# Performance work log

Measured on AMD Instinct MI355X. Metric: run time of the kernel, lower is better.

Reference implementation:

```python
import jax, jax.numpy as jnp
import numpy as np

DIM = 512
HID = 512
H = 8
HD = HID // H
RB_HID = 64
COORD = 3


def setup_inputs() -> dict:
    key = jax.random.key(0)
    ks = jax.random.split(key, 12)
    B, Nq, Nk = 2, 1024, 2048
    s = 0.02
    return {
        "q_in": jax.random.normal(ks[0], (B, Nq, DIM), jnp.float32),
        "kv_in": jax.random.normal(ks[1], (B, Nk, DIM), jnp.float32),
        "q_coords": jax.random.normal(ks[2], (B, Nq, COORD), jnp.float32),
        "kv_coords": jax.random.normal(ks[3], (B, Nk, COORD), jnp.float32),
        "Wq": jax.random.normal(ks[4], (DIM, HID), jnp.float32) * s,
        "Wk": jax.random.normal(ks[5], (DIM, HID), jnp.float32) * s,
        "Wv": jax.random.normal(ks[6], (DIM, HID), jnp.float32) * s,
        "Wo": jax.random.normal(ks[7], (HID, DIM), jnp.float32) * s,
        "W1": jax.random.normal(ks[8], (1, RB_HID), jnp.float32) * s,
        "b1": jnp.zeros((RB_HID,), jnp.float32),
        "W2": jax.random.normal(ks[9], (RB_HID, H), jnp.float32) * s,
        "b2": jnp.zeros((H,), jnp.float32),
    }


def reference(q_in, kv_in, q_coords, kv_coords, Wq, Wk, Wv, Wo, W1, b1, W2, b2):
    B, Nq, _ = q_in.shape
    Nk = kv_in.shape[1]
    # projections -> [B, H, N, HD]
    q = (q_in @ Wq).reshape(B, Nq, H, HD).transpose(0, 2, 1, 3)
    k = (kv_in @ Wk).reshape(B, Nk, H, HD).transpose(0, 2, 1, 3)
    v = (kv_in @ Wv).reshape(B, Nk, H, HD).transpose(0, 2, 1, 3)
    # pairwise Euclidean distance [B, Nq, Nk]
    diff = q_coords[:, :, None, :] - kv_coords[:, None, :, :]
    d = jnp.sqrt(jnp.sum(diff * diff, axis=-1))
    # 2-layer MLP on distance -> per-head bias [B, H, Nq, Nk]
    h = jax.nn.silu(d[..., None] * W1[0] + b1)  # [B,Nq,Nk,RB_HID]
    bias = (h @ W2 + b2).transpose(0, 3, 1, 2)  # [B,H,Nq,Nk]
    scale = HD ** -0.5
    logits = jnp.einsum("bhqd,bhkd->bhqk", q, k) * scale + bias
    attn = jax.nn.softmax(logits, axis=-1)
    out = jnp.einsum("bhqk,bhkd->bhqd", attn, v)
    out = out.transpose(0, 2, 1, 3).reshape(B, Nq, HID)
    return out @ Wo
```

## Files before the change

### kernel.cpp

```cpp
#include <hip/hip_runtime.h>
#include <hip/hip_bf16.h>
#include <math.h>

typedef short bf16x8 __attribute__((ext_vector_type(8)));
typedef float f32x4 __attribute__((ext_vector_type(4)));
typedef unsigned short u16;
typedef unsigned int u32;

#define NH 8
#define BB 2
#define NQ 1024
#define NK 2048
#define M2CONST 6.4921250
#define SC2 0.18033688f

#define MFMA16(a, b, c) __builtin_amdgcn_mfma_f32_16x16x32_bf16(a, b, c, 0, 0, 0)

__device__ __constant__ double XN_D[6] = {15.727406610312546, 13.656854249492380,
                                          10.070552360820166, 5.9294476391798335,
                                          2.3431457505076194, 0.27259338968745405};
#define XN0 15.727406610312546f
#define XN1 13.656854249492380f
#define XN2 10.070552360820166f
#define XN3 5.9294476391798335f
#define XN4 2.3431457505076194f

static __device__ __forceinline__ u16 f2us(float x) {
  union { __hip_bfloat16 b; u16 u; } cv;
  cv.b = __float2bfloat16(x);
  return cv.u;
}

static __device__ __forceinline__ u32 bfr(float x) {
  u32 u = __builtin_bit_cast(u32, x);
  return u + 0x7FFFu + ((u >> 16) & 1u);
}
static __device__ __forceinline__ u32 pk2(float lo, float hi) {
  return (bfr(lo) >> 16) | (bfr(hi) & 0xFFFF0000u);
}
static __device__ __forceinline__ u16 bfs(float x) { return (u16)(bfr(x) >> 16); }

static __device__ __forceinline__ bf16x8 pack8(float4 a, float4 b) {
  union { bf16x8 v; uint4 u; } cv;
  cv.u.x = pk2(a.x, a.y);
  cv.u.y = pk2(a.z, a.w);
  cv.u.z = pk2(b.x, b.y);
  cv.u.w = pk2(b.z, b.w);
  return cv.v;
}

__global__ __launch_bounds__(256) void setup_kernel(
    const float* __restrict__ Wq, const float* __restrict__ Wk,
    const float* __restrict__ Wv, const float* __restrict__ Wo,
    u16* __restrict__ Tq, u16* __restrict__ Tk,
    u16* __restrict__ Tv, u16* __restrict__ To,
    const float* __restrict__ W1, const float* __restrict__ b1,
    const float* __restrict__ W2, const float* __restrict__ b2,
    float* __restrict__ polyc,
    const float* __restrict__ kc, u16* __restrict__ keg) {
  const int blk = blockIdx.x, t = threadIdx.x;
  if (blk < 256) {
    __shared__ u16 tile[64][65];
    const float* W; u16* Wt;
    switch (blk >> 6) {
      case 0: W = Wq; Wt = Tq; break;
      case 1: W = Wk; Wt = Tk; break;
      case 2: W = Wv; Wt = Tv; break;
      default: W = Wo; Wt = To; break;
    }
    const int rem = blk & 63;
    const int k0 = (rem >> 3) * 64, n0 = (rem & 7) * 64;
    const int r = t >> 4, c4 = (t & 15) * 4;
    #pragma unroll
    for (int p = 0; p < 4; p++) {
      int row = p * 16 + r;
      float4 v = *(const float4*)&W[(size_t)(k0 + row) * 512 + n0 + c4];
      tile[row][c4 + 0] = f2us(v.x);
      tile[row][c4 + 1] = f2us(v.y);
      tile[row][c4 + 2] = f2us(v.z);
      tile[row][c4 + 3] = f2us(v.w);
    }
    __syncthreads();
    #pragma unroll
    for (int p = 0; p < 4; p++) {
      int n = p * 16 + r;
      u16 u0 = tile[c4 + 0][n], u1 = tile[c4 + 1][n];
      u16 u2 = tile[c4 + 2][n], u3 = tile[c4 + 3][n];
      uint2 o;
      o.x = u0 | ((u32)u1 << 16);
      o.y = u2 | ((u32)u3 << 16);
      *(uint2*)&Wt[(size_t)(n0 + n) * 512 + k0 + c4] = o;
    }
  } else if (blk == 256) {
    __shared__ double fv[6][8];
    if (t < 48) {
      int i = t >> 3, h = t & 7;
      double x = XN_D[i];
      double acc = (double)b2[h];
      for (int r = 0; r < 64; r++) {
        double u = x * (double)W1[r] + (double)b1[r];
        double s = u / (1.0 + exp(-u));
        acc += s * (double)W2[r * 8 + h];
      }
      fv[i][h] = acc * 1.4426950408889634 - M2CONST;
    }
    __syncthreads();
    if (t < 8) {
      int h = t;
      double c[6];
      #pragma unroll
      for (int i = 0; i < 6; i++) c[i] = fv[i][h];
      for (int k = 1; k < 6; k++)
        for (int i = 5; i >= k; i--)
          c[i] = (c[i] - c[i - 1]) / (XN_D[i] - XN_D[i - k]);
      #pragma unroll
      for (int j = 0; j < 6; j++) polyc[h * 8 + j] = (float)c[j];
    }
  } else {
    int r = (blk - 257) * 256 + t;
    float kx = kc[(size_t)r * 3], ky = kc[(size_t)r * 3 + 1], kz = kc[(size_t)r * 3 + 2];
    uint4 o;
    o.x = f2us(-2.0f * kx) | ((u32)f2us(-2.0f * ky) << 16);
    o.y = f2us(-2.0f * kz) | ((u32)f2us(1.0f) << 16);
    o.z = (u32)f2us(kx * kx + ky * ky + kz * kz);
    o.w = 0;
    *(uint4*)&keg[(size_t)r * 8] = o;
  }
}

__global__ __launch_bounds__(256) void gemm_qkv(
    const float* __restrict__ q_in, const float* __restrict__ kv_in,
    const u16* __restrict__ Wqt, const u16* __restrict__ Wkt,
    const u16* __restrict__ Wvt, u16* __restrict__ Qp,
    u16* __restrict__ Kp, u16* __restrict__ Vtp) {
  __shared__ u16 As[64 * 72];
  __shared__ u16 Bs[64 * 72];
  __shared__ u16 Bs2[64 * 72];
  const int t = threadIdx.x;
  const int w = t >> 6, l = t & 63, g = l >> 4, li = l & 15;
  const int bx = blockIdx.x;
  const bool isQ = bx < 32;
  const int m0 = (isQ ? bx : bx - 32) * 64, n0 = blockIdx.y * 64;
  const float* A = isQ ? q_in : kv_in;
  const u16* B1 = isQ ? Wqt : Wkt;
  const int ms = (w & 1) * 32, ns = (w >> 1) * 32;
  const int ar = t >> 2, ac = (t & 3) * 16;
  f32x4 acc[2][2] = {}, accV[2][2] = {};

  for (int kt = 0; kt < 512; kt += 64) {
    float4 a4[4];
    #pragma unroll
    for (int q = 0; q < 4; q++)
      a4[q] = *(const float4*)&A[(size_t)(m0 + ar) * 512 + kt + ac + 4 * q];
    bf16x8 bk[2], bv2[2];
    #pragma unroll
    for (int p = 0; p < 2; p++) {
      int f = p * 256 + t, r = f >> 3, c8 = (f & 7) * 8;
      bk[p] = *(const bf16x8*)&B1[(size_t)(n0 + r) * 512 + kt + c8];
    }
    if (!isQ) {
      #pragma unroll
      for (int p = 0; p < 2; p++) {
        int f = p * 256 + t, r = f >> 3, c8 = (f & 7) * 8;
        bv2[p] = *(const bf16x8*)&Wvt[(size_t)(n0 + r) * 512 + kt + c8];
      }
    }
    __syncthreads();
    *(bf16x8*)&As[ar * 72 + ac] = pack8(a4[0], a4[1]);
    *(bf16x8*)&As[ar * 72 + ac + 8] = pack8(a4[2], a4[3]);
    #pragma unroll
    for (int p = 0; p < 2; p++) {
      int f = p * 256 + t, r = f >> 3, c8 = (f & 7) * 8;
      *(bf16x8*)&Bs[r * 72 + c8] = bk[p];
    }
    if (!isQ) {
      #pragma unroll
      for (int p = 0; p < 2; p++) {
        int f = p * 256 + t, r = f >> 3, c8 = (f & 7) * 8;
        *(bf16x8*)&Bs2[r * 72 + c8] = bv2[p];
      }
    }
    __syncthreads();
    #pragma unroll
    for (int ks = 0; ks < 2; ks++) {
      bf16x8 a0 = *(const bf16x8*)&As[(ms + li) * 72 + ks * 32 + g * 8];
      bf16x8 a1 = *(const bf16x8*)&As[(ms + 16 + li) * 72 + ks * 32 + g * 8];
      bf16x8 k0 = *(const bf16x8*)&Bs[(ns + li) * 72 + ks * 32 + g * 8];
      bf16x8 k1 = *(const bf16x8*)&Bs[(ns + 16 + li) * 72 + ks * 32 + g * 8];
      acc[0][0] = MFMA16(a0, k0, acc[0][0]);
      acc[0][1] = MFMA16(a0, k1, acc[0][1]);
      acc[1][0] = MFMA16(a1, k0, acc[1][0]);
      acc[1][1] = MFMA16(a1, k1, acc[1][1]);
      if (!isQ) {
        bf16x8 v0 = *(const bf16x8*)&Bs2[(ns + li) * 72 + ks * 32 + g * 8];
        bf16x8 v1 = *(const bf16x8*)&Bs2[(ns + 16 + li) * 72 + ks * 32 + g * 8];
        accV[0][0] = MFMA16(a0, v0, accV[0][0]);
        accV[0][1] = MFMA16(a0, v1, accV[0][1]);
        accV[1][0] = MFMA16(a1, v0, accV[1][0]);
        accV[1][1] = MFMA16(a1, v1, accV[1][1]);
      }
    }
  }
  #pragma unroll
  for (int mi = 0; mi < 2; mi++) {
    #pragma unroll
    for (int ni = 0; ni < 2; ni++) {
      int row = m0 + ms + mi * 16 + 4 * g;
      int col = n0 + ns + ni * 16 + li;
      f32x4 vk = acc[mi][ni];
      if (isQ) {
        #pragma unroll
        for (int r = 0; r < 4; r++) Qp[(size_t)(row + r) * 512 + col] = bfs(vk[r]);
      } else {
        #pragma unroll
        for (int r = 0; r < 4; r++) Kp[(size_t)(row + r) * 512 + col] = bfs(vk[r]);
        f32x4 vv = accV[mi][ni];
        int bb = row >> 11, j = row & 2047;
        int hh = col >> 6, d = col & 63;
        uint2 o;
        o.x = pk2(vv[0], vv[1]);
        o.y = pk2(vv[2], vv[3]);
        *(uint2*)&Vtp[((size_t)((bb * 8 + hh) * 64 + d)) * 2048 + j] = o;
      }
    }
  }
}

__global__ __launch_bounds__(256, 4) void attn_kernel(
    const u16* __restrict__ Qb, const u16* __restrict__ Kb,
    const u16* __restrict__ Vt, const float* __restrict__ qc,
    const u16* __restrict__ keg, const float* __restrict__ polyc,
    float* __restrict__ Op, float* __restrict__ Lp) {
  __shared__ u16 Kl[64 * 72];
  __shared__ u16 Vtl[64 * 72];
  __shared__ u16 Pl[64 * 72];

  const int t = threadIdx.x;
  const int w = t >> 6, l = t & 63, g = l >> 4, li = l & 15;
  const int qt = blockIdx.x >> 2, sidx = blockIdx.x & 3;
  const int h = blockIdx.y, b = blockIdx.z;

  const float c0 = polyc[h * 8 + 0], c1 = polyc[h * 8 + 1];
  const float c2 = polyc[h * 8 + 2], c3 = polyc[h * 8 + 3];
  const float c4 = polyc[h * 8 + 4], c5 = polyc[h * 8 + 5];

  const int qrow = qt * 64 + w * 16 + li;
  const size_t qg = (size_t)b * NQ + qrow;
  bf16x8 qf0 = *(const bf16x8*)&Qb[qg * 512 + h * 64 + g * 8];
  bf16x8 qf1 = *(const bf16x8*)&Qb[qg * 512 + h * 64 + 32 + g * 8];
  float qx = qc[qg * 3], qy = qc[qg * 3 + 1], qz = qc[qg * 3 + 2];
  bf16x8 qe = {};
  if (g == 0) {
    qe[0] = (short)f2us(qx);
    qe[1] = (short)f2us(qy);
    qe[2] = (short)f2us(qz);
    qe[3] = (short)f2us(qx * qx + qy * qy + qz * qz);
    qe[4] = (short)f2us(1.0f);
  }

  f32x4 oacc[4] = {};
  float lacc = 0.0f;

  const u16* Kg = Kb + (size_t)b * NK * 512 + h * 64;
  const u16* Vg = Vt + (size_t)((b * 8 + h) * 64) * 2048;
  const u16* keg_b = keg + (size_t)b * NK * 8;

  for (int it = 0; it < 8; it++) {
    const int jbase = sidx * 512 + it * 64;
    __syncthreads();
    #pragma unroll
    for (int pp = 0; pp < 2; pp++) {
      int f = pp * 256 + t, row = f >> 3, c8 = (f & 7) * 8;
      *(bf16x8*)&Kl[row * 72 + c8] =
          *(const bf16x8*)&Kg[(size_t)(jbase + row) * 512 + c8];
      *(bf16x8*)&Vtl[row * 72 + c8] =
          *(const bf16x8*)&Vg[(size_t)row * 2048 + jbase + c8];
    }
    __syncthreads();

    f32x4 sac[4], dac[4];
    #pragma unroll
    for (int j4 = 0; j4 < 4; j4++) {
      bf16x8 ka0 = *(const bf16x8*)&Kl[(j4 * 16 + li) * 72 + g * 8];
      bf16x8 ka1 = *(const bf16x8*)&Kl[(j4 * 16 + li) * 72 + 32 + g * 8];
      f32x4 z = {};
      f32x4 s0 = MFMA16(ka0, qf0, z);
      sac[j4] = MFMA16(ka1, qf1, s0);
      bf16x8 ke = {};
      if (g == 0)
        ke = *(const bf16x8*)&keg_b[(size_t)(jbase + j4 * 16 + li) * 8];
      dac[j4] = MFMA16(ke, qe, z);
    }

    #pragma unroll
    for (int j4 = 0; j4 < 4; j4++) {
      float p[4];
      #pragma unroll
      for (int r = 0; r < 4; r++) {
        float u = fmaxf(dac[j4][r], 0.0f);
        float d = fminf(__builtin_amdgcn_sqrtf(u), 16.0f);
        float gp = c5;
        gp = fmaf(gp, d - XN4, c4);
        gp = fmaf(gp, d - XN3, c3);
        gp = fmaf(gp, d - XN2, c2);
        gp = fmaf(gp, d - XN1, c1);
        gp = fmaf(gp, d - XN0, c0);
        p[r] = __builtin_amdgcn_exp2f(fmaf(sac[j4][r], SC2, gp));
        lacc += p[r];
      }
      uint2 pv;
      pv.x = pk2(p[0], p[1]);
      pv.y = pk2(p[2], p[3]);
      *(uint2*)&Pl[(w * 16 + li) * 72 + j4 * 16 + g * 4] = pv;
    }

    bf16x8 pf0 = *(const bf16x8*)&Pl[(w * 16 + li) * 72 + g * 8];
    bf16x8 pf1 = *(const bf16x8*)&Pl[(w * 16 + li) * 72 + 32 + g * 8];
    #pragma unroll
    for (int dt = 0; dt < 4; dt++) {
      bf16x8 v0 = *(const bf16x8*)&Vtl[(dt * 16 + li) * 72 + g * 8];
      bf16x8 v1 = *(const bf16x8*)&Vtl[(dt * 16 + li) * 72 + 32 + g * 8];
      oacc[dt] = MFMA16(pf0, v0, oacc[dt]);
      oacc[dt] = MFMA16(pf1, v1, oacc[dt]);
    }
  }

  float lf = lacc;
  lf += __shfl_xor(lf, 16);
  lf += __shfl_xor(lf, 32);

  const size_t obase =
      ((size_t)(sidx * 16 + b * 8 + h) * 1024 + qt * 64 + w * 16) * 64;
  #pragma unroll
  for (int dt = 0; dt < 4; dt++)
    #pragma unroll
    for (int r = 0; r < 4; r++)
      Op[obase + (size_t)(4 * g + r) * 64 + dt * 16 + li] = oacc[dt][r];
  if (g == 0)
    Lp[(size_t)(sidx * 16 + b * 8 + h) * 1024 + qt * 64 + w * 16 + li] = lf;
}

__global__ __launch_bounds__(256) void gemm_wo(const float* __restrict__ Op,
                                               const float* __restrict__ Lp,
                                               const u16* __restrict__ Bt,
                                               float* __restrict__ C) {
  __shared__ u16 As[32 * 72];
  __shared__ u16 Bs[64 * 72];
  const int t = threadIdx.x;
  const int w = t >> 6, l = t & 63, g = l >> 4, li = l & 15;
  const int m0 = blockIdx.x * 32, n0 = blockIdx.y * 64;
  const int ms = (w & 1) * 16, ns = (w >> 1) * 32;
  const int arow = t >> 3, ac8 = (t & 7) * 8;
  const int bq = (m0 + arow) >> 10, qrow = (m0 + arow) & 1023;
  f32x4 acc[2] = {};

  for (int kt = 0; kt < 512; kt += 64) {
    const int h = kt >> 6;
    const int bh = bq * 8 + h;
    f32x4 s0 = {}, s1 = {};
    float lsum = 0.0f;
    #pragma unroll
    for (int s = 0; s < 4; s++) {
      const float* base = &Op[((size_t)(s * 16 + bh) * 1024 + qrow) * 64 + ac8];
      s0 += *(const f32x4*)base;
      s1 += *(const f32x4*)(base + 4);
      lsum += Lp[(size_t)(s * 16 + bh) * 1024 + qrow];
    }
    float inv = __builtin_amdgcn_rcpf(lsum);
    bf16x8 bv[2];
    #pragma unroll
    for (int p = 0; p < 2; p++) {
      int f = p * 256 + t, r = f >> 3, c8 = (f & 7) * 8;
      bv[p] = *(const bf16x8*)&Bt[(size_t)(n0 + r) * 512 + kt + c8];
    }
    __syncthreads();
    {
      union { bf16x8 v; uint4 u; } cv;
      cv.u.x = pk2(s0[0] * inv, s0[1] * inv);
      cv.u.y = pk2(s0[2] * inv, s0[3] * inv);
      cv.u.z = pk2(s1[0] * inv, s1[1] * inv);
      cv.u.w = pk2(s1[2] * inv, s1[3] * inv);
      *(bf16x8*)&As[arow * 72 + ac8] = cv.v;
    }
    #pragma unroll
    for (int p = 0; p < 2; p++) {
      int f = p * 256 + t, r = f >> 3, c8 = (f & 7) * 8;
      *(bf16x8*)&Bs[r * 72 + c8] = bv[p];
    }
    __syncthreads();
    #pragma unroll
    for (int ks = 0; ks < 2; ks++) {
      bf16x8 af = *(const bf16x8*)&As[(ms + li) * 72 + ks * 32 + g * 8];
      bf16x8 b0 = *(const bf16x8*)&Bs[(ns + li) * 72 + ks * 32 + g * 8];
      bf16x8 b1 = *(const bf16x8*)&Bs[(ns + 16 + li) * 72 + ks * 32 + g * 8];
      acc[0] = MFMA16(af, b0, acc[0]);
      acc[1] = MFMA16(af, b1, acc[1]);
    }
  }
  #pragma unroll
  for (int ni = 0; ni < 2; ni++) {
    f32x4 v = acc[ni];
    int row = m0 + ms + 4 * g;
    int col = n0 + ns + ni * 16 + li;
    #pragma unroll
    for (int r = 0; r < 4; r++) C[(size_t)(row + r) * 512 + col] = v[r];
  }
}

extern "C" void kernel_launch(void* const* d_in, const int* in_sizes, int n_in,
                              void* d_out, int out_size, void* d_ws, size_t ws_size,
                              hipStream_t stream) {
  const float* q_in      = (const float*)d_in[0];
  const float* kv_in     = (const float*)d_in[1];
  const float* q_coords  = (const float*)d_in[2];
  const float* kv_coords = (const float*)d_in[3];
  const float* Wq        = (const float*)d_in[4];
  const float* Wk        = (const float*)d_in[5];
  const float* Wv        = (const float*)d_in[6];
  const float* Wo        = (const float*)d_in[7];
  const float* W1        = (const float*)d_in[8];
  const float* b1        = (const float*)d_in[9];
  const float* W2        = (const float*)d_in[10];
  const float* b2        = (const float*)d_in[11];

  char* p = (char*)d_ws;
  u16* Wqt  = (u16*)p; p += (size_t)512 * 512 * 2;
  u16* Wkt  = (u16*)p; p += (size_t)512 * 512 * 2;
  u16* Wvt  = (u16*)p; p += (size_t)512 * 512 * 2;
  u16* Wot  = (u16*)p; p += (size_t)512 * 512 * 2;
  u16* Qp   = (u16*)p; p += (size_t)2048 * 512 * 2;
  u16* Kp   = (u16*)p; p += (size_t)4096 * 512 * 2;
  u16* Vtp  = (u16*)p; p += (size_t)4096 * 512 * 2;
  u16* keg  = (u16*)p; p += (size_t)4096 * 8 * 2;
  float* polyc = (float*)p; p += (size_t)64 * 4;
  p = (char*)(((size_t)p + 255) & ~(size_t)255);
  float* Opart = (float*)p; p += (size_t)4 * 16 * 1024 * 64 * 4;
  float* Lpart = (float*)p; p += (size_t)4 * 16 * 1024 * 4;

  setup_kernel<<<273, 256, 0, stream>>>(Wq, Wk, Wv, Wo, Wqt, Wkt, Wvt, Wot,
                                        W1, b1, W2, b2, polyc, kv_coords, keg);
  gemm_qkv<<<dim3(96, 8), 256, 0, stream>>>(q_in, kv_in, Wqt, Wkt, Wvt,
                                            Qp, Kp, Vtp);
  attn_kernel<<<dim3(64, 8, 2), 256, 0, stream>>>(Qp, Kp, Vtp, q_coords, keg,
                                                  polyc, Opart, Lpart);
  gemm_wo<<<dim3(64, 8), 256, 0, stream>>>(Opart, Lpart, Wot, (float*)d_out);
}
```

Measured before the change: 152.7 us.

## Double attention KV split and move partial combine into a separate kernel

The attention kernel now splits the KV range 8 ways instead of 4, doubling the grid, and raises its occupancy hint from 4 to 6. The merge of partial outputs is moved out of the Wo GEMM into a new combine kernel that writes normalized bf16 activations, which the GEMM then reads directly. LDS row stride drops from 72 to 68 elements and bf16 conversions switch to a custom rounding helper. The extra kernel launch, the larger fp32 partial buffers and the added reduction traffic are the costs paid for the higher parallelism.

```diff
diff --git a/kernel.cpp b/kernel.cpp
--- a/kernel.cpp
+++ b/kernel.cpp
@@ -11,8 +11,10 @@
 #define BB 2
 #define NQ 1024
 #define NK 2048
+#define NSPLIT 8
 #define M2CONST 6.4921250
 #define SC2 0.18033688f
+#define LS 68
 
 #define MFMA16(a, b, c) __builtin_amdgcn_mfma_f32_16x16x32_bf16(a, b, c, 0, 0, 0)
 
@@ -24,12 +26,6 @@
 #define XN2 10.070552360820166f
 #define XN3 5.9294476391798335f
 #define XN4 2.3431457505076194f
-
-static __device__ __forceinline__ u16 f2us(float x) {
-  union { __hip_bfloat16 b; u16 u; } cv;
-  cv.b = __float2bfloat16(x);
-  return cv.u;
-}
 
 static __device__ __forceinline__ u32 bfr(float x) {
   u32 u = __builtin_bit_cast(u32, x);
@@ -75,10 +71,10 @@
     for (int p = 0; p < 4; p++) {
       int row = p * 16 + r;
       float4 v = *(const float4*)&W[(size_t)(k0 + row) * 512 + n0 + c4];
-      tile[row][c4 + 0] = f2us(v.x);
-      tile[row][c4 + 1] = f2us(v.y);
-      tile[row][c4 + 2] = f2us(v.z);
-      tile[row][c4 + 3] = f2us(v.w);
+      tile[row][c4 + 0] = bfs(v.x);
+      tile[row][c4 + 1] = bfs(v.y);
+      tile[row][c4 + 2] = bfs(v.z);
+      tile[row][c4 + 3] = bfs(v.w);
     }
     __syncthreads();
     #pragma unroll
@@ -120,9 +116,9 @@
     int r = (blk - 257) * 256 + t;
     float kx = kc[(size_t)r * 3], ky = kc[(size_t)r * 3 + 1], kz = kc[(size_t)r * 3 + 2];
     uint4 o;
-    o.x = f2us(-2.0f * kx) | ((u32)f2us(-2.0f * ky) << 16);
-    o.y = f2us(-2.0f * kz) | ((u32)f2us(1.0f) << 16);
-    o.z = (u32)f2us(kx * kx + ky * ky + kz * kz);
+    o.x = pk2(-2.0f * kx, -2.0f * ky);
+    o.y = pk2(-2.0f * kz, 1.0f);
+    o.z = (u32)bfs(kx * kx + ky * ky + kz * kz);
     o.w = 0;
     *(uint4*)&keg[(size_t)r * 8] = o;
   }
@@ -133,9 +129,9 @@
     const u16* __restrict__ Wqt, const u16* __restrict__ Wkt,
     const u16* __restrict__ Wvt, u16* __restrict__ Qp,
     u16* __restrict__ Kp, u16* __restrict__ Vtp) {
-  __shared__ u16 As[64 * 72];
-  __shared__ u16 Bs[64 * 72];
-  __shared__ u16 Bs2[64 * 72];
+  __shared__ u16 As[64 * LS];
+  __shared__ u16 Bs[64 * LS];
+  __shared__ u16 Bs2[64 * LS];
   const int t = threadIdx.x;
   const int w = t >> 6, l = t & 63, g = l >> 4, li = l & 15;
   const int bx = blockIdx.x;
@@ -166,34 +162,34 @@
       }
     }
     __syncthreads();
-    *(bf16x8*)&As[ar * 72 + ac] = pack8(a4[0], a4[1]);
-    *(bf16x8*)&As[ar * 72 + ac + 8] = pack8(a4[2], a4[3]);
+    *(bf16x8*)&As[ar * LS + ac] = pack8(a4[0], a4[1]);
+    *(bf16x8*)&As[ar * LS + ac + 8] = pack8(a4[2], a4[3]);
     #pragma unroll
     for (int p = 0; p < 2; p++) {
       int f = p * 256 + t, r = f >> 3, c8 = (f & 7) * 8;
-      *(bf16x8*)&Bs[r * 72 + c8] = bk[p];
+      *(bf16x8*)&Bs[r * LS + c8] = bk[p];
     }
     if (!isQ) {
       #pragma unroll
       for (int p = 0; p < 2; p++) {
         int f = p * 256 + t, r = f >> 3, c8 = (f & 7) * 8;
-        *(bf16x8*)&Bs2[r * 72 + c8] = bv2[p];
+        *(bf16x8*)&Bs2[r * LS + c8] = bv2[p];
       }
     }
     __syncthreads();
     #pragma unroll
     for (int ks = 0; ks < 2; ks++) {
-      bf16x8 a0 = *(const bf16x8*)&As[(ms + li) * 72 + ks * 32 + g * 8];
-      bf16x8 a1 = *(const bf16x8*)&As[(ms + 16 + li) * 72 + ks * 32 + g * 8];
-      bf16x8 k0 = *(const bf16x8*)&Bs[(ns + li) * 72 + ks * 32 + g * 8];
-      bf16x8 k1 = *(const bf16x8*)&Bs[(ns + 16 + li) * 72 + ks * 32 + g * 8];
+      bf16x8 a0 = *(const bf16x8*)&As[(ms + li) * LS + ks * 32 + g * 8];
+      bf16x8 a1 = *(const bf16x8*)&As[(ms + 16 + li) * LS + ks * 32 + g * 8];
+      bf16x8 k0 = *(const bf16x8*)&Bs[(ns + li) * LS + ks * 32 + g * 8];
+      bf16x8 k1 = *(const bf16x8*)&Bs[(ns + 16 + li) * LS + ks * 32 + g * 8];
       acc[0][0] = MFMA16(a0, k0, acc[0][0]);
       acc[0][1] = MFMA16(a0, k1, acc[0][1]);
       acc[1][0] = MFMA16(a1, k0, acc[1][0]);
       acc[1][1] = MFMA16(a1, k1, acc[1][1]);
       if (!isQ) {
-        bf16x8 v0 = *(const bf16x8*)&Bs2[(ns + li) * 72 + ks * 32 + g * 8];
-        bf16x8 v1 = *(const bf16x8*)&Bs2[(ns + 16 + li) * 72 + ks * 32 + g * 8];
+        bf16x8 v0 = *(const bf16x8*)&Bs2[(ns + li) * LS + ks * 32 + g * 8];
+        bf16x8 v1 = *(const bf16x8*)&Bs2[(ns + 16 + li) * LS + ks * 32 + g * 8];
         accV[0][0] = MFMA16(a0, v0, accV[0][0]);
         accV[0][1] = MFMA16(a0, v1, accV[0][1]);
         accV[1][0] = MFMA16(a1, v0, accV[1][0]);
@@ -226,18 +222,18 @@
   }
 }
 
-__global__ __launch_bounds__(256, 4) void attn_kernel(
+__global__ __launch_bounds__(256, 6) void attn_kernel(
     const u16* __restrict__ Qb, const u16* __restrict__ Kb,
     const u16* __restrict__ Vt, const float* __restrict__ qc,
     const u16* __restrict__ keg, const float* __restrict__ polyc,
     float* __restrict__ Op, float* __restrict__ Lp) {
-  __shared__ u16 Kl[64 * 72];
-  __shared__ u16 Vtl[64 * 72];
-  __shared__ u16 Pl[64 * 72];
+  __shared__ u16 Kl[64 * LS];
+  __shared__ u16 Vtl[64 * LS];
+  __shared__ u16 Pl[64 * LS];
 
   const int t = threadIdx.x;
   const int w = t >> 6, l = t & 63, g = l >> 4, li = l & 15;
-  const int qt = blockIdx.x >> 2, sidx = blockIdx.x & 3;
+  const int qt = blockIdx.x >> 3, sidx = blockIdx.x & 7;
   const int h = blockIdx.y, b = blockIdx.z;
 
   const float c0 = polyc[h * 8 + 0], c1 = polyc[h * 8 + 1];
@@ -251,11 +247,11 @@
   float qx = qc[qg * 3], qy = qc[qg * 3 + 1], qz = qc[qg * 3 + 2];
   bf16x8 qe = {};
   if (g == 0) {
-    qe[0] = (short)f2us(qx);
-    qe[1] = (short)f2us(qy);
-    qe[2] = (short)f2us(qz);
-    qe[3] = (short)f2us(qx * qx + qy * qy + qz * qz);
-    qe[4] = (short)f2us(1.0f);
+    qe[0] = (short)bfs(qx);
+    qe[1] = (short)bfs(qy);
+    qe[2] = (short)bfs(qz);
+    qe[3] = (short)bfs(qx * qx + qy * qy + qz * qz);
+    qe[4] = (short)bfs(1.0f);
   }
 
   f32x4 oacc[4] = {};
@@ -265,15 +261,15 @@
   const u16* Vg = Vt + (size_t)((b * 8 + h) * 64) * 2048;
   const u16* keg_b = keg + (size_t)b * NK * 8;
 
-  for (int it = 0; it < 8; it++) {
-    const int jbase = sidx * 512 + it * 64;
+  for (int it = 0; it < NK / NSPLIT / 64; it++) {
+    const int jbase = sidx * (NK / NSPLIT) + it * 64;
     __syncthreads();
     #pragma unroll
     for (int pp = 0; pp < 2; pp++) {
       int f = pp * 256 + t, row = f >> 3, c8 = (f & 7) * 8;
-      *(bf16x8*)&Kl[row * 72 + c8] =
+      *(bf16x8*)&Kl[row * LS + c8] =
           *(const bf16x8*)&Kg[(size_t)(jbase + row) * 512 + c8];
-      *(bf16x8*)&Vtl[row * 72 + c8] =
+      *(bf16x8*)&Vtl[row * LS + c8] =
           *(const bf16x8*)&Vg[(size_t)row * 2048 + jbase + c8];
     }
     __syncthreads();
@@ -281,8 +277,8 @@
     f32x4 sac[4], dac[4];
     #pragma unroll
     for (int j4 = 0; j4 < 4; j4++) {
-      bf16x8 ka0 = *(const bf16x8*)&Kl[(j4 * 16 + li) * 72 + g * 8];
-      bf16x8 ka1 = *(const bf16x8*)&Kl[(j4 * 16 + li) * 72 + 32 + g * 8];
+      bf16x8 ka0 = *(const bf16x8*)&Kl[(j4 * 16 + li) * LS + g * 8];
+      bf16x8 ka1 = *(const bf16x8*)&Kl[(j4 * 16 + li) * LS + 32 + g * 8];
       f32x4 z = {};
       f32x4 s0 = MFMA16(ka0, qf0, z);
       sac[j4] = MFMA16(ka1, qf1, s0);
@@ -311,15 +307,15 @@
       uint2 pv;
       pv.x = pk2(p[0], p[1]);
       pv.y = pk2(p[2], p[3]);
-      *(uint2*)&Pl[(w * 16 + li) * 72 + j4 * 16 + g * 4] = pv;
-    }
-
-    bf16x8 pf0 = *(const bf16x8*)&Pl[(w * 16 + li) * 72 + g * 8];
-    bf16x8 pf1 = *(const bf16x8*)&Pl[(w * 16 + li) * 72 + 32 + g * 8];
+      *(uint2*)&Pl[(w * 16 + li) * LS + j4 * 16 + g * 4] = pv;
+    }
+
+    bf16x8 pf0 = *(const bf16x8*)&Pl[(w * 16 + li) * LS + g * 8];
+    bf16x8 pf1 = *(const bf16x8*)&Pl[(w * 16 + li) * LS + 32 + g * 8];
     #pragma unroll
     for (int dt = 0; dt < 4; dt++) {
-      bf16x8 v0 = *(const bf16x8*)&Vtl[(dt * 16 + li) * 72 + g * 8];
-      bf16x8 v1 = *(const bf16x8*)&Vtl[(dt * 16 + li) * 72 + 32 + g * 8];
+      bf16x8 v0 = *(const bf16x8*)&Vtl[(dt * 16 + li) * LS + g * 8];
+      bf16x8 v1 = *(const bf16x8*)&Vtl[(dt * 16 + li) * LS + 32 + g * 8];
       oacc[dt] = MFMA16(pf0, v0, oacc[dt]);
       oacc[dt] = MFMA16(pf1, v1, oacc[dt]);
     }
@@ -340,34 +336,43 @@
     Lp[(size_t)(sidx * 16 + b * 8 + h) * 1024 + qt * 64 + w * 16 + li] = lf;
 }
 
-__global__ __launch_bounds__(256) void gemm_wo(const float* __restrict__ Op,
-                                               const float* __restrict__ Lp,
+__global__ __launch_bounds__(256) void combine_kernel(const float* __restrict__ Op,
+                                                      const float* __restrict__ Lp,
+                                                      u16* __restrict__ AOb) {
+  int tid = blockIdx.x * 256 + threadIdx.x;
+  int d4 = tid & 15, rh = tid >> 4;
+  int bh = rh >> 10, qrow = rh & 1023;
+  f32x4 o = {};
+  float lsum = 0.0f;
+  #pragma unroll
+  for (int s = 0; s < NSPLIT; s++) {
+    f32x4 v = *(const f32x4*)&Op[((size_t)(s * 16 + bh) * 1024 + qrow) * 64 + d4 * 4];
+    o += v;
+    lsum += Lp[(size_t)(s * 16 + bh) * 1024 + qrow];
+  }
+  float inv = __builtin_amdgcn_rcpf(lsum);
+  uint2 pk;
+  pk.x = pk2(o[0] * inv, o[1] * inv);
+  pk.y = pk2(o[2] * inv, o[3] * inv);
+  *(uint2*)&AOb[((size_t)(bh >> 3) * NQ + qrow) * 512 + (bh & 7) * 64 + d4 * 4] = pk;
+}
+
+__global__ __launch_bounds__(256) void gemm_wo(const u16* __restrict__ A,
                                                const u16* __restrict__ Bt,
                                                float* __restrict__ C) {
-  __shared__ u16 As[32 * 72];
-  __shared__ u16 Bs[64 * 72];
+  __shared__ u16 As[32 * LS];
+  __shared__ u16 Bs[64 * LS];
   const int t = threadIdx.x;
   const int w = t >> 6, l = t & 63, g = l >> 4, li = l & 15;
   const int m0 = blockIdx.x * 32, n0 = blockIdx.y * 64;
   const int ms = (w & 1) * 16, ns = (w >> 1) * 32;
-  const int arow = t >> 3, ac8 = (t & 7) * 8;
-  const int bq = (m0 + arow) >> 10, qrow = (m0 + arow) & 1023;
   f32x4 acc[2] = {};
-
   for (int kt = 0; kt < 512; kt += 64) {
-    const int h = kt >> 6;
-    const int bh = bq * 8 + h;
-    f32x4 s0 = {}, s1 = {};
-    float lsum = 0.0f;
-    #pragma unroll
-    for (int s = 0; s < 4; s++) {
-      const float* base = &Op[((size_t)(s * 16 + bh) * 1024 + qrow) * 64 + ac8];
-      s0 += *(const f32x4*)base;
-      s1 += *(const f32x4*)(base + 4);
-      lsum += Lp[(size_t)(s * 16 + bh) * 1024 + qrow];
-    }
-    float inv = __builtin_amdgcn_rcpf(lsum);
-    bf16x8 bv[2];
+    bf16x8 av, bv[2];
+    {
+      int r = t >> 3, c8 = (t & 7) * 8;
+      av = *(const bf16x8*)&A[(size_t)(m0 + r) * 512 + kt + c8];
+    }
     #pragma unroll
     for (int p = 0; p < 2; p++) {
       int f = p * 256 + t, r = f >> 3, c8 = (f & 7) * 8;
@@ -375,24 +380,20 @@
     }
     __syncthreads();
     {
-      union { bf16x8 v; uint4 u; } cv;
-      cv.u.x = pk2(s0[0] * inv, s0[1] * inv);
-      cv.u.y = pk2(s0[2] * inv, s0[3] * inv);
-      cv.u.z = pk2(s1[0] * inv, s1[1] * inv);
-      cv.u.w = pk2(s1[2] * inv, s1[3] * inv);
-      *(bf16x8*)&As[arow * 72 + ac8] = cv.v;
+      int r = t >> 3, c8 = (t & 7) * 8;
+      *(bf16x8*)&As[r * LS + c8] = av;
     }
     #pragma unroll
     for (int p = 0; p < 2; p++) {
       int f = p * 256 + t, r = f >> 3, c8 = (f & 7) * 8;
-      *(bf16x8*)&Bs[r * 72 + c8] = bv[p];
+      *(bf16x8*)&Bs[r * LS + c8] = bv[p];
     }
     __syncthreads();
     #pragma unroll
     for (int ks = 0; ks < 2; ks++) {
-      bf16x8 af = *(const bf16x8*)&As[(ms + li) * 72 + ks * 32 + g * 8];
-      bf16x8 b0 = *(const bf16x8*)&Bs[(ns + li) * 72 + ks * 32 + g * 8];
-      bf16x8 b1 = *(const bf16x8*)&Bs[(ns + 16 + li) * 72 + ks * 32 + g * 8];
+      bf16x8 af = *(const bf16x8*)&As[(ms + li) * LS + ks * 32 + g * 8];
+      bf16x8 b0 = *(const bf16x8*)&Bs[(ns + li) * LS + ks * 32 + g * 8];
+      bf16x8 b1 = *(const bf16x8*)&Bs[(ns + 16 + li) * LS + ks * 32 + g * 8];
       acc[0] = MFMA16(af, b0, acc[0]);
       acc[1] = MFMA16(af, b1, acc[1]);
     }
@@ -431,17 +432,19 @@
   u16* Qp   = (u16*)p; p += (size_t)2048 * 512 * 2;
   u16* Kp   = (u16*)p; p += (size_t)4096 * 512 * 2;
   u16* Vtp  = (u16*)p; p += (size_t)4096 * 512 * 2;
+  u16* AOb  = (u16*)p; p += (size_t)2048 * 512 * 2;
   u16* keg  = (u16*)p; p += (size_t)4096 * 8 * 2;
   float* polyc = (float*)p; p += (size_t)64 * 4;
   p = (char*)(((size_t)p + 255) & ~(size_t)255);
-  float* Opart = (float*)p; p += (size_t)4 * 16 * 1024 * 64 * 4;
-  float* Lpart = (float*)p; p += (size_t)4 * 16 * 1024 * 4;
+  float* Opart = (float*)p; p += (size_t)NSPLIT * 16 * 1024 * 64 * 4;
+  float* Lpart = (float*)p; p += (size_t)NSPLIT * 16 * 1024 * 4;
 
   setup_kernel<<<273, 256, 0, stream>>>(Wq, Wk, Wv, Wo, Wqt, Wkt, Wvt, Wot,
                                         W1, b1, W2, b2, polyc, kv_coords, keg);
   gemm_qkv<<<dim3(96, 8), 256, 0, stream>>>(q_in, kv_in, Wqt, Wkt, Wvt,
                                             Qp, Kp, Vtp);
-  attn_kernel<<<dim3(64, 8, 2), 256, 0, stream>>>(Qp, Kp, Vtp, q_coords, keg,
-                                                  polyc, Opart, Lpart);
-  gemm_wo<<<dim3(64, 8), 256, 0, stream>>>(Opart, Lpart, Wot, (float*)d_out);
-}
+  attn_kernel<<<dim3(128, 8, 2), 256, 0, stream>>>(Qp, Kp, Vtp, q_coords, keg,
+                                                   polyc, Opart, Lpart);
+  combine_kernel<<<1024, 256, 0, stream>>>(Opart, Lpart, AOb);
+  gemm_wo<<<dim3(64, 8), 256, 0, stream>>>(AOb, Wot, (float*)d_out);
+}
```

Measured after the change: 153.2 us. About the same (+0.3%).
